# Performance work log

Measured on AMD Instinct MI355X. Metric: run time of the kernel, lower is better.

## Reference

```python
import jax, jax.numpy as jnp
import numpy as np


def _topk_axis(x, k, axis, largest):
    # lax.top_k works on the last axis, largest, sorted descending.
    xm = jnp.moveaxis(x, axis, -1)
    if largest:
        vals, idx = jax.lax.top_k(xm, k)
    else:
        vals, idx = jax.lax.top_k(-xm, k)
        vals = -vals  # ascending smallest-k, matching torch.topk(largest=False, sorted=True)
    return jnp.moveaxis(vals, -1, axis), jnp.moveaxis(idx, -1, axis)


def setup_inputs() -> dict:
    key = jax.random.key(0)
    k0, k1, k2 = jax.random.split(key, 3)
    v_0 = jax.random.normal(k0, (4096, 32000), dtype=jnp.float32)
    v_1 = jax.random.normal(k1, (8, 16, 64, 4096), dtype=jnp.float32)
    v_2 = jax.random.normal(k2, (100000, 512), dtype=jnp.float32)
    return {"v_0": v_0, "v_1": v_1, "v_2": v_2}


def reference(v_0, v_1, v_2):
    # TopK_0: k=2, dim=1, largest, sorted
    v_4, v_5 = _topk_axis(v_0, 2, 1, largest=True)
    # TopK_1: k=4, dim=3, smallest, sorted
    v_7, v_8 = _topk_axis(v_1, 4, 3, largest=False)
    # TopK_2: k=3, dim=0, largest, sorted
    v_10, v_11 = _topk_axis(v_2, 3, 0, largest=True)
    return (v_4, v_5, v_7, v_8, v_10, v_11)
```

## Files before the change

kernel.cpp:

```cpp
#include <hip/hip_runtime.h>
#include <limits.h>
#include <math.h>

typedef unsigned long long u64;
typedef unsigned int u32;

__device__ __forceinline__ u32 f2ord(float v) {
    u32 u = __float_as_uint(v);
    return (u & 0x80000000u) ? ~u : (u | 0x80000000u);
}
__device__ __forceinline__ float ord2f(u32 s) {
    u32 u = (s & 0x80000000u) ? (s & 0x7FFFFFFFu) : ~s;
    return __uint_as_float(u);
}
__device__ __forceinline__ u64 keylg(float v, u32 i) { return ((u64)f2ord(v) << 32) | (u64)(~i); }
__device__ __forceinline__ u64 keysm(float v, u32 i) { return ((u64)f2ord(v) << 32) | (u64)i; }
__device__ __forceinline__ float val_of(u64 k) { return ord2f((u32)(k >> 32)); }
__device__ __forceinline__ float idxf_lg(u64 k) { return (float)(~(u32)k); }
__device__ __forceinline__ float idxf_sm(u64 k) { return (float)((u32)k); }

__device__ __forceinline__ u64 mx64(u64 a, u64 b) { return a > b ? a : b; }
__device__ __forceinline__ u64 mn64(u64 a, u64 b) { return a < b ? a : b; }

__device__ __forceinline__ void ins2_lg(u64& s0, u64& s1, u64 k) {
    u64 t0 = mx64(s0, k), r0 = mn64(s0, k);
    s0 = t0; s1 = mx64(s1, r0);
}
__device__ __forceinline__ void ins3_lg(u64& s0, u64& s1, u64& s2, u64 k) {
    u64 t0 = mx64(s0, k), r0 = mn64(s0, k);
    u64 t1 = mx64(s1, r0), r1 = mn64(s1, r0);
    s0 = t0; s1 = t1; s2 = mx64(s2, r1);
}
__device__ __forceinline__ void ins4_sm(u64& s0, u64& s1, u64& s2, u64& s3, u64 k) {
    u64 t0 = mn64(s0, k), r0 = mx64(s0, k);
    u64 t1 = mn64(s1, r0), r1 = mx64(s1, r0);
    u64 t2 = mn64(s2, r1), r2 = mx64(s2, r1);
    s0 = t0; s1 = t1; s2 = t2; s3 = mn64(s3, r2);
}

__device__ __forceinline__ void ce_max(u64& a, u64& b) { u64 h = mx64(a, b), l = mn64(a, b); a = h; b = l; }
__device__ __forceinline__ void ce_min(u64& a, u64& b) { u64 l = mn64(a, b), h = mx64(a, b); a = l; b = h; }

__device__ __forceinline__ void merge2_lg(u64& a0, u64& a1, u64 b0, u64 b1) {
    u64 l0 = mx64(a0, b1), l1 = mx64(a1, b0);
    a0 = mx64(l0, l1); a1 = mn64(l0, l1);
}
__device__ __forceinline__ void merge3_lg(u64& a0, u64& a1, u64& a2, u64 b0, u64 b1, u64 b2) {
    u64 l0 = mx64(a0, b2), l1 = mx64(a1, b1), l2 = mx64(a2, b0);
    ce_max(l0, l1); ce_max(l1, l2); ce_max(l0, l1);
    a0 = l0; a1 = l1; a2 = l2;
}
__device__ __forceinline__ void merge4_sm(u64& a0, u64& a1, u64& a2, u64& a3,
                                          u64 b0, u64 b1, u64 b2, u64 b3) {
    u64 l0 = mn64(a0, b3), l1 = mn64(a1, b2), l2 = mn64(a2, b1), l3 = mn64(a3, b0);
    ce_min(l0, l2); ce_min(l1, l3); ce_min(l0, l1); ce_min(l2, l3);
    a0 = l0; a1 = l1; a2 = l2; a3 = l3;
}

__device__ __forceinline__ u64 shx64(u64 v, int m) {
    u32 hi = __shfl_xor((u32)(v >> 32), m);
    u32 lo = __shfl_xor((u32)v, m);
    return ((u64)hi << 32) | (u64)lo;
}

__global__ __launch_bounds__(256) void mega_kernel(
    const float* __restrict__ x0, float* __restrict__ o0v, float* __restrict__ o0i,
    const float* __restrict__ x1, float* __restrict__ o1v, float* __restrict__ o1i,
    const float* __restrict__ x2, u64* __restrict__ part, int rpb, int do_p1)
{
    const int bid  = blockIdx.x;
    const int wave = threadIdx.x >> 6;
    const int lane = threadIdx.x & 63;

    if (bid < 512) {
        if (!do_p1) return;
        const int blk = bid;
        const int c0  = threadIdx.x * 2;
        int rbeg = blk * rpb;
        int rend = rbeg + rpb; if (rend > 100000) rend = 100000;

        u64 a0 = 0, a1 = 0, a2 = 0;
        u64 b0 = 0, b1 = 0, b2 = 0;

#define P1LOAD(r) (*(const float2*)(x2 + (size_t)(r) * 512 + c0))
#define P1UPD(f, rr) \
        ins3_lg(a0, a1, a2, keylg((f).x, (u32)(rr))); \
        ins3_lg(b0, b1, b2, keylg((f).y, (u32)(rr)))

        int r = rbeg;
        for (; r + 3 < rend; r += 4) {
            float2 f0 = P1LOAD(r);
            float2 f1 = P1LOAD(r + 1);
            float2 f2 = P1LOAD(r + 2);
            float2 f3 = P1LOAD(r + 3);
            P1UPD(f0, r); P1UPD(f1, r + 1); P1UPD(f2, r + 2); P1UPD(f3, r + 3);
        }
        for (; r < rend; ++r) {
            float2 f0 = P1LOAD(r);
            P1UPD(f0, r);
        }
#undef P1LOAD
#undef P1UPD

        u64* base = part + (size_t)blk * 1536;
        base[0 * 512 + c0] = a0; base[0 * 512 + c0 + 1] = b0;
        base[1 * 512 + c0] = a1; base[1 * 512 + c0 + 1] = b1;
        base[2 * 512 + c0] = a2; base[2 * 512 + c0 + 1] = b2;

    } else if (bid < 1536) {
        const int row = (bid - 512) * 4 + wave;
        const float4* xr = (const float4*)(x0 + (size_t)row * 32000);
        u64 s0 = 0, s1 = 0;

#define K0UPD(f, b) \
        ins2_lg(s0, s1, keylg((f).x, (u32)(b)));     \
        ins2_lg(s0, s1, keylg((f).y, (u32)(b) + 1)); \
        ins2_lg(s0, s1, keylg((f).z, (u32)(b) + 2)); \
        ins2_lg(s0, s1, keylg((f).w, (u32)(b) + 3))

        int v = lane;
        for (int it = 0; it < 31; ++it, v += 256) {
            float4 t0 = xr[v];
            float4 t1 = xr[v + 64];
            float4 t2 = xr[v + 128];
            float4 t3 = xr[v + 192];
            K0UPD(t0, v * 4); K0UPD(t1, (v + 64) * 4);
            K0UPD(t2, (v + 128) * 4); K0UPD(t3, (v + 192) * 4);
        }
        { float4 t = xr[v]; K0UPD(t, v * 4); }
#undef K0UPD

        for (int m = 1; m < 64; m <<= 1) {
            u64 b0 = shx64(s0, m), b1 = shx64(s1, m);
            merge2_lg(s0, s1, b0, b1);
        }
        if (lane == 0) {
            o0v[row * 2 + 0] = val_of(s0);  o0v[row * 2 + 1] = val_of(s1);
            o0i[row * 2 + 0] = idxf_lg(s0); o0i[row * 2 + 1] = idxf_lg(s1);
        }

    } else {
        const int row = (bid - 1536) * 4 + wave;
        const float4* xr = (const float4*)(x1 + (size_t)row * 4096);
        u64 s0 = ~0ull, s1 = ~0ull, s2 = ~0ull, s3 = ~0ull;

#define K1UPD(f, b) \
        ins4_sm(s0, s1, s2, s3, keysm((f).x, (u32)(b)));     \
        ins4_sm(s0, s1, s2, s3, keysm((f).y, (u32)(b) + 1)); \
        ins4_sm(s0, s1, s2, s3, keysm((f).z, (u32)(b) + 2)); \
        ins4_sm(s0, s1, s2, s3, keysm((f).w, (u32)(b) + 3))

        int v = lane;
        for (int it = 0; it < 4; ++it, v += 256) {
            float4 t0 = xr[v];
            float4 t1 = xr[v + 64];
            float4 t2 = xr[v + 128];
            float4 t3 = xr[v + 192];
            K1UPD(t0, v * 4); K1UPD(t1, (v + 64) * 4);
            K1UPD(t2, (v + 128) * 4); K1UPD(t3, (v + 192) * 4);
        }
#undef K1UPD

        for (int m = 1; m < 64; m <<= 1) {
            u64 b0 = shx64(s0, m), b1 = shx64(s1, m);
            u64 b2 = shx64(s2, m), b3 = shx64(s3, m);
            merge4_sm(s0, s1, s2, s3, b0, b1, b2, b3);
        }
        if (lane == 0) {
            o1v[row * 4 + 0] = val_of(s0);  o1v[row * 4 + 1] = val_of(s1);
            o1v[row * 4 + 2] = val_of(s2);  o1v[row * 4 + 3] = val_of(s3);
            o1i[row * 4 + 0] = idxf_sm(s0); o1i[row * 4 + 1] = idxf_sm(s1);
            o1i[row * 4 + 2] = idxf_sm(s2); o1i[row * 4 + 3] = idxf_sm(s3);
        }
    }
}

__global__ __launch_bounds__(256) void topk2_reduce(
    const u64* __restrict__ part, float* __restrict__ outv, float* __restrict__ outi)
{
    const int wave = threadIdx.x >> 6;
    const int lane = threadIdx.x & 63;
    const int col  = blockIdx.x * 4 + wave;

    u64 a0 = 0, a1 = 0, a2 = 0;
#pragma unroll
    for (int j = 0; j < 8; ++j) {
        const u64* q = part + (size_t)(lane + 64 * j) * 1536 + col;
        merge3_lg(a0, a1, a2, q[0], q[512], q[1024]);
    }
    for (int m = 1; m < 64; m <<= 1) {
        u64 b0 = shx64(a0, m), b1 = shx64(a1, m), b2 = shx64(a2, m);
        merge3_lg(a0, a1, a2, b0, b1, b2);
    }

    if (lane == 0) {
        outv[0 * 512 + col] = val_of(a0);
        outv[1 * 512 + col] = val_of(a1);
        outv[2 * 512 + col] = val_of(a2);
        outi[0 * 512 + col] = idxf_lg(a0);
        outi[1 * 512 + col] = idxf_lg(a1);
        outi[2 * 512 + col] = idxf_lg(a2);
    }
}

__global__ __launch_bounds__(256) void topk2_direct(
    const float* __restrict__ x, float* __restrict__ outv, float* __restrict__ outi)
{
    const int col = blockIdx.x * 256 + threadIdx.x;
    u64 a0 = 0, a1 = 0, a2 = 0;
    for (int r = 0; r < 100000; ++r) {
        float v = x[(size_t)r * 512 + col];
        ins3_lg(a0, a1, a2, keylg(v, (u32)r));
    }
    outv[0 * 512 + col] = val_of(a0);
    outv[1 * 512 + col] = val_of(a1);
    outv[2 * 512 + col] = val_of(a2);
    outi[0 * 512 + col] = idxf_lg(a0);
    outi[1 * 512 + col] = idxf_lg(a1);
    outi[2 * 512 + col] = idxf_lg(a2);
}

extern "C" void kernel_launch(void* const* d_in, const int* in_sizes, int n_in,
                              void* d_out, int out_size, void* d_ws, size_t ws_size,
                              hipStream_t stream) {
    const float* v0 = (const float*)d_in[0];
    const float* v1 = (const float*)d_in[1];
    const float* v2 = (const float*)d_in[2];
    float* out = (float*)d_out;

    float* o_v4  = out;
    float* o_v5  = out + 8192;
    float* o_v7  = out + 16384;
    float* o_v8  = out + 49152;
    float* o_v10 = out + 81920;
    float* o_v11 = out + 83456;

    const int NB = 512;
    int rpb = (100000 + NB - 1) / NB;
    size_t need = (size_t)NB * 3 * 512 * sizeof(u64);

    if (ws_size >= need) {
        u64* part = (u64*)d_ws;
        mega_kernel<<<3584, 256, 0, stream>>>(v0, o_v4, o_v5,
                                              v1, o_v7, o_v8,
                                              v2, part, rpb, 1);
        topk2_reduce<<<128, 256, 0, stream>>>(part, o_v10, o_v11);
    } else {
        mega_kernel<<<3584, 256, 0, stream>>>(v0, o_v4, o_v5,
                                              v1, o_v7, o_v8,
                                              v2, (u64*)d_ws, rpb, 0);
        topk2_direct<<<2, 256, 0, stream>>>(v2, o_v10, o_v11);
    }
}
```

Baseline: 178.3 us.

## Use small sorting networks per float4, reorder block roles, unroll column scan

Replaces per-element insertion into the running top-k with a small network that first sorts or selects within each float4 and then bitonic-merges into the running state. The top-2 path splits its state into two independent accumulators to shorten dependency chains. The block-role order is swapped so the heavy top-2 row blocks are dispatched first, and the column-scan loop is unrolled from 4 to 8 loads. The float-to-ordered-key conversion becomes branchless. The aim is to cut 64-bit compare/select ALU work and raise memory-level parallelism, at the cost of more registers.

Measured after the change: 171.1 us. -4.1%, faster.

```diff
diff --git a/kernel.cpp b/kernel.cpp
--- a/kernel.cpp
+++ b/kernel.cpp
@@ -7,7 +7,7 @@
 
 __device__ __forceinline__ u32 f2ord(float v) {
     u32 u = __float_as_uint(v);
-    return (u & 0x80000000u) ? ~u : (u | 0x80000000u);
+    return u ^ (((u32)((int)u >> 31)) | 0x80000000u);
 }
 __device__ __forceinline__ float ord2f(u32 s) {
     u32 u = (s & 0x80000000u) ? (s & 0x7FFFFFFFu) : ~s;
@@ -22,20 +22,10 @@
 __device__ __forceinline__ u64 mx64(u64 a, u64 b) { return a > b ? a : b; }
 __device__ __forceinline__ u64 mn64(u64 a, u64 b) { return a < b ? a : b; }
 
-__device__ __forceinline__ void ins2_lg(u64& s0, u64& s1, u64 k) {
-    u64 t0 = mx64(s0, k), r0 = mn64(s0, k);
-    s0 = t0; s1 = mx64(s1, r0);
-}
 __device__ __forceinline__ void ins3_lg(u64& s0, u64& s1, u64& s2, u64 k) {
     u64 t0 = mx64(s0, k), r0 = mn64(s0, k);
     u64 t1 = mx64(s1, r0), r1 = mn64(s1, r0);
     s0 = t0; s1 = t1; s2 = mx64(s2, r1);
-}
-__device__ __forceinline__ void ins4_sm(u64& s0, u64& s1, u64& s2, u64& s3, u64 k) {
-    u64 t0 = mn64(s0, k), r0 = mx64(s0, k);
-    u64 t1 = mn64(s1, r0), r1 = mx64(s1, r0);
-    u64 t2 = mn64(s2, r1), r2 = mx64(s2, r1);
-    s0 = t0; s1 = t1; s2 = t2; s3 = mn64(s3, r2);
 }
 
 __device__ __forceinline__ void ce_max(u64& a, u64& b) { u64 h = mx64(a, b), l = mn64(a, b); a = h; b = l; }
@@ -61,6 +51,26 @@
     u32 hi = __shfl_xor((u32)(v >> 32), m);
     u32 lo = __shfl_xor((u32)v, m);
     return ((u64)hi << 32) | (u64)lo;
+}
+
+__device__ __forceinline__ void top2of4_lg(float4 f, u32 b, u64& o0, u64& o1) {
+    u64 k0 = keylg(f.x, b), k1 = keylg(f.y, b + 1);
+    u64 k2 = keylg(f.z, b + 2), k3 = keylg(f.w, b + 3);
+    u64 h0 = mx64(k0, k1), l0 = mn64(k0, k1);
+    u64 h1 = mx64(k2, k3), l1 = mn64(k2, k3);
+    u64 m0 = mx64(h0, l1), m1 = mx64(l0, h1);
+    o0 = mx64(m0, m1); o1 = mn64(m0, m1);
+}
+
+__device__ __forceinline__ void sort4_sm(float4 f, u32 bse,
+                                         u64& b0, u64& b1, u64& b2, u64& b3) {
+    u64 k0 = keysm(f.x, bse), k1 = keysm(f.y, bse + 1);
+    u64 k2 = keysm(f.z, bse + 2), k3 = keysm(f.w, bse + 3);
+    u64 p0 = mn64(k0, k1), p1 = mx64(k0, k1);
+    u64 q0 = mn64(k2, k3), q1 = mx64(k2, k3);
+    b0 = mn64(p0, q0); u64 t = mx64(p0, q0);
+    b3 = mx64(p1, q1); u64 u = mn64(p1, q1);
+    b1 = mn64(t, u); b2 = mx64(t, u);
 }
 
 __global__ __launch_bounds__(256) void mega_kernel(
@@ -72,51 +82,10 @@
     const int wave = threadIdx.x >> 6;
     const int lane = threadIdx.x & 63;
 
-    if (bid < 512) {
-        if (!do_p1) return;
-        const int blk = bid;
-        const int c0  = threadIdx.x * 2;
-        int rbeg = blk * rpb;
-        int rend = rbeg + rpb; if (rend > 100000) rend = 100000;
-
-        u64 a0 = 0, a1 = 0, a2 = 0;
-        u64 b0 = 0, b1 = 0, b2 = 0;
-
-#define P1LOAD(r) (*(const float2*)(x2 + (size_t)(r) * 512 + c0))
-#define P1UPD(f, rr) \
-        ins3_lg(a0, a1, a2, keylg((f).x, (u32)(rr))); \
-        ins3_lg(b0, b1, b2, keylg((f).y, (u32)(rr)))
-
-        int r = rbeg;
-        for (; r + 3 < rend; r += 4) {
-            float2 f0 = P1LOAD(r);
-            float2 f1 = P1LOAD(r + 1);
-            float2 f2 = P1LOAD(r + 2);
-            float2 f3 = P1LOAD(r + 3);
-            P1UPD(f0, r); P1UPD(f1, r + 1); P1UPD(f2, r + 2); P1UPD(f3, r + 3);
-        }
-        for (; r < rend; ++r) {
-            float2 f0 = P1LOAD(r);
-            P1UPD(f0, r);
-        }
-#undef P1LOAD
-#undef P1UPD
-
-        u64* base = part + (size_t)blk * 1536;
-        base[0 * 512 + c0] = a0; base[0 * 512 + c0 + 1] = b0;
-        base[1 * 512 + c0] = a1; base[1 * 512 + c0 + 1] = b1;
-        base[2 * 512 + c0] = a2; base[2 * 512 + c0 + 1] = b2;
-
-    } else if (bid < 1536) {
-        const int row = (bid - 512) * 4 + wave;
+    if (bid < 1024) {
+        const int row = bid * 4 + wave;
         const float4* xr = (const float4*)(x0 + (size_t)row * 32000);
-        u64 s0 = 0, s1 = 0;
-
-#define K0UPD(f, b) \
-        ins2_lg(s0, s1, keylg((f).x, (u32)(b)));     \
-        ins2_lg(s0, s1, keylg((f).y, (u32)(b) + 1)); \
-        ins2_lg(s0, s1, keylg((f).z, (u32)(b) + 2)); \
-        ins2_lg(s0, s1, keylg((f).w, (u32)(b) + 3))
+        u64 sA0 = 0, sA1 = 0, sB0 = 0, sB1 = 0;
 
         int v = lane;
         for (int it = 0; it < 31; ++it, v += 256) {
@@ -124,31 +93,76 @@
             float4 t1 = xr[v + 64];
             float4 t2 = xr[v + 128];
             float4 t3 = xr[v + 192];
-            K0UPD(t0, v * 4); K0UPD(t1, (v + 64) * 4);
-            K0UPD(t2, (v + 128) * 4); K0UPD(t3, (v + 192) * 4);
-        }
-        { float4 t = xr[v]; K0UPD(t, v * 4); }
-#undef K0UPD
+            u64 w0, w1;
+            top2of4_lg(t0, (u32)(v * 4),         w0, w1); merge2_lg(sA0, sA1, w0, w1);
+            top2of4_lg(t1, (u32)((v + 64) * 4),  w0, w1); merge2_lg(sB0, sB1, w0, w1);
+            top2of4_lg(t2, (u32)((v + 128) * 4), w0, w1); merge2_lg(sA0, sA1, w0, w1);
+            top2of4_lg(t3, (u32)((v + 192) * 4), w0, w1); merge2_lg(sB0, sB1, w0, w1);
+        }
+        {
+            float4 t = xr[v];
+            u64 w0, w1;
+            top2of4_lg(t, (u32)(v * 4), w0, w1); merge2_lg(sA0, sA1, w0, w1);
+        }
+        merge2_lg(sA0, sA1, sB0, sB1);
 
         for (int m = 1; m < 64; m <<= 1) {
-            u64 b0 = shx64(s0, m), b1 = shx64(s1, m);
-            merge2_lg(s0, s1, b0, b1);
+            u64 b0 = shx64(sA0, m), b1 = shx64(sA1, m);
+            merge2_lg(sA0, sA1, b0, b1);
         }
         if (lane == 0) {
-            o0v[row * 2 + 0] = val_of(s0);  o0v[row * 2 + 1] = val_of(s1);
-            o0i[row * 2 + 0] = idxf_lg(s0); o0i[row * 2 + 1] = idxf_lg(s1);
-        }
+            o0v[row * 2 + 0] = val_of(sA0);  o0v[row * 2 + 1] = val_of(sA1);
+            o0i[row * 2 + 0] = idxf_lg(sA0); o0i[row * 2 + 1] = idxf_lg(sA1);
+        }
+
+    } else if (bid < 1536) {
+        if (!do_p1) return;
+        const int blk = bid - 1024;
+        const int c0  = threadIdx.x * 2;
+        int rbeg = blk * rpb;
+        int rend = rbeg + rpb; if (rend > 100000) rend = 100000;
+
+        u64 a0 = 0, a1 = 0, a2 = 0;
+        u64 b0 = 0, b1 = 0, b2 = 0;
+
+#define P1LOAD(r) (*(const float2*)(x2 + (size_t)(r) * 512 + c0))
+#define P1UPD(f, rr) \
+        ins3_lg(a0, a1, a2, keylg((f).x, (u32)(rr))); \
+        ins3_lg(b0, b1, b2, keylg((f).y, (u32)(rr)))
+
+        int r = rbeg;
+        for (; r + 7 < rend; r += 8) {
+            float2 f0 = P1LOAD(r);
+            float2 f1 = P1LOAD(r + 1);
+            float2 f2 = P1LOAD(r + 2);
+            float2 f3 = P1LOAD(r + 3);
+            float2 f4 = P1LOAD(r + 4);
+            float2 f5 = P1LOAD(r + 5);
+            float2 f6 = P1LOAD(r + 6);
+            float2 f7 = P1LOAD(r + 7);
+            P1UPD(f0, r);     P1UPD(f1, r + 1); P1UPD(f2, r + 2); P1UPD(f3, r + 3);
+            P1UPD(f4, r + 4); P1UPD(f5, r + 5); P1UPD(f6, r + 6); P1UPD(f7, r + 7);
+        }
+        for (; r < rend; ++r) {
+            float2 f0 = P1LOAD(r);
+            P1UPD(f0, r);
+        }
+#undef P1LOAD
+#undef P1UPD
+
+        u64* base = part + (size_t)blk * 1536;
+        base[0 * 512 + c0] = a0; base[0 * 512 + c0 + 1] = b0;
+        base[1 * 512 + c0] = a1; base[1 * 512 + c0 + 1] = b1;
+        base[2 * 512 + c0] = a2; base[2 * 512 + c0 + 1] = b2;
 
     } else {
         const int row = (bid - 1536) * 4 + wave;
         const float4* xr = (const float4*)(x1 + (size_t)row * 4096);
         u64 s0 = ~0ull, s1 = ~0ull, s2 = ~0ull, s3 = ~0ull;
 
-#define K1UPD(f, b) \
-        ins4_sm(s0, s1, s2, s3, keysm((f).x, (u32)(b)));     \
-        ins4_sm(s0, s1, s2, s3, keysm((f).y, (u32)(b) + 1)); \
-        ins4_sm(s0, s1, s2, s3, keysm((f).z, (u32)(b) + 2)); \
-        ins4_sm(s0, s1, s2, s3, keysm((f).w, (u32)(b) + 3))
+#define K1UPD(f, b) { u64 c0_, c1_, c2_, c3_;                      \
+        sort4_sm((f), (u32)(b), c0_, c1_, c2_, c3_);               \
+        merge4_sm(s0, s1, s2, s3, c0_, c1_, c2_, c3_); }
 
         int v = lane;
         for (int it = 0; it < 4; ++it, v += 256) {
@@ -156,8 +170,10 @@
             float4 t1 = xr[v + 64];
             float4 t2 = xr[v + 128];
             float4 t3 = xr[v + 192];
-            K1UPD(t0, v * 4); K1UPD(t1, (v + 64) * 4);
-            K1UPD(t2, (v + 128) * 4); K1UPD(t3, (v + 192) * 4);
+            K1UPD(t0, v * 4);
+            K1UPD(t1, (v + 64) * 4);
+            K1UPD(t2, (v + 128) * 4);
+            K1UPD(t3, (v + 192) * 4);
         }
 #undef K1UPD
 
```
